# Kernel tuning notes

Measured on AMD Instinct MI355X. Metric: run time of the kernel, lower is better.

The kernel has to match this reference:

```python
import jax, jax.numpy as jnp
import numpy as np

N, E, F, O = 50000, 800000, 128, 128
LOW = [0, 1, 2, 4]           # single-radius (low-pass) channels
BAND = [(0, 1), (1, 2), (2, 4)]  # two-radius (band-pass) channels
KMAX = 4


def setup_inputs() -> dict:
    key = jax.random.key(0)
    ks = jax.random.split(key, 16)
    x = jax.random.normal(ks[0], (N, F), dtype=jnp.float32)
    # edges with no self-loops (dst = src + offset mod N, offset in [1, N))
    src = jax.random.randint(ks[1], (E,), 0, N)
    off = jax.random.randint(ks[2], (E,), 1, N)
    dst = (src + off) % N
    edge_index = jnp.stack([src, dst]).astype(jnp.int64)
    s_lin = 1.0 / np.sqrt(F)
    s_att = 1.0 / np.sqrt(O)
    W_low = jax.random.normal(ks[3], (len(LOW), F, O), jnp.float32) * s_lin
    b_low = jnp.zeros((len(LOW), O), jnp.float32)
    W_band = jax.random.normal(ks[4], (len(BAND), F, O), jnp.float32) * s_lin
    b_band = jnp.zeros((len(BAND), O), jnp.float32)
    att_pre_low = jax.random.normal(ks[5], (1, O), jnp.float32) * s_att
    att_channel_low = jax.random.normal(ks[6], (1, O), jnp.float32) * s_att
    att_pre_band = jax.random.normal(ks[7], (1, O), jnp.float32) * s_att
    att_channel_band = jax.random.normal(ks[8], (1, O), jnp.float32) * s_att
    W_mlp = jax.random.normal(ks[9], (2 * O, O), jnp.float32) * (1.0 / np.sqrt(2 * O))
    b_mlp = jnp.zeros((O,), jnp.float32)
    return {"x": x, "edge_index": edge_index, "W_low": W_low, "b_low": b_low,
            "W_band": W_band, "b_band": b_band,
            "att_pre_low": att_pre_low, "att_channel_low": att_channel_low,
            "att_pre_band": att_pre_band, "att_channel_band": att_channel_band,
            "W_mlp": W_mlp, "b_mlp": b_mlp}


def _sym_norm_weights(src, dst, n, dtype):
    # degree over edges WITHOUT self-loops; self-loop weight is 1, all / 2
    deg = jax.ops.segment_sum(jnp.ones(src.shape[0], dtype), dst, num_segments=n)
    d_inv_sqrt = jnp.where(deg > 0, 1.0 / jnp.sqrt(jnp.maximum(deg, 1e-12)), 0.0)
    return d_inv_sqrt[src] * d_inv_sqrt[dst] * 0.5  # [E]; self-loop coeff is 0.5


def _propagate(x, src, dst, w, n):
    # out[i] = sum_{e: dst=i} w_e * x[src_e] + 0.5 * x[i]  (self-loop term)
    msg = x[src] * w[:, None]  # [E, O]
    return jax.ops.segment_sum(msg, dst, num_segments=n) + 0.5 * x


def _att_combine(h, att_pre, att_ch):
    # h: [C, N, O]; single head attention over channels
    a = jax.nn.relu(h)
    h_pre = a.mean(axis=0)  # [N, O]
    logits = jax.nn.relu(h_pre @ att_pre[0] + jnp.einsum('cno,o->cn', a, att_ch[0]))
    alpha = jax.nn.softmax(logits, axis=0)  # softmax over channels
    return jnp.einsum('cn,cno->no', alpha, h)


def reference(x, edge_index, W_low, b_low, W_band, b_band,
              att_pre_low, att_channel_low, att_pre_band, att_channel_band,
              W_mlp, b_mlp):
    src, dst = edge_index[0], edge_index[1]
    n = x.shape[0]
    w = _sym_norm_weights(src, dst, n, x.dtype)
    # K-hop propagation, store aggregates at required radii
    aggs = {0: x}
    a = x
    for k in range(1, KMAX + 1):
        a = _propagate(a, src, dst, w, n)
        aggs[k] = a
    feats_low = jnp.stack([aggs[k] for k in LOW])                     # [Cl, N, F]
    feats_band = jnp.stack([aggs[k1] - aggs[k2] for k1, k2 in BAND])  # [Cb, N, F]
    h_low = jnp.einsum('cnf,cfo->cno', feats_low, W_low) + b_low[:, None, :]
    h_band = jnp.einsum('cnf,cfo->cno', feats_band, W_band) + b_band[:, None, :]
    out_low = _att_combine(h_low, att_pre_low, att_channel_low)
    out_band = _att_combine(h_band, att_pre_band, att_channel_band)
    out = jnp.concatenate([out_low, out_band], axis=-1) @ W_mlp + b_mlp
    return out
```

## Files before the change

kernel.cpp:

```cpp
#include <hip/hip_runtime.h>
#include <math.h>

#define NN 50000
#define NE 800000
#define TM 16
#define NPAN 4
#define PSZ 12500
#define NT (NN * NPAN)
#define SCH 1024
#define NSB ((NT + SCH - 1) / SCH)

typedef _Float16 half4v __attribute__((ext_vector_type(4)));
typedef _Float16 half8v __attribute__((ext_vector_type(8)));
typedef float f32x4 __attribute__((ext_vector_type(4)));

__device__ __forceinline__ float relu(float v) { return fmaxf(v, 0.0f); }

__global__ __launch_bounds__(256) void k_deg2(const int* __restrict__ ei,
                                              int* __restrict__ deg2) {
  int e = blockIdx.x * 256 + threadIdx.x;
  if (e < NE) {
    int s = ei[e];
    int d = ei[NE + e];
    atomicAdd(&deg2[d * NPAN + s / PSZ], 1);
  }
}

__global__ __launch_bounds__(256) void k_dinv(const int* __restrict__ deg2,
                                              float* __restrict__ dinv) {
  int i = blockIdx.x * 256 + threadIdx.x;
  if (i < NN) {
    int d = deg2[i * NPAN] + deg2[i * NPAN + 1] + deg2[i * NPAN + 2] +
            deg2[i * NPAN + 3];
    dinv[i] = d > 0 ? 1.0f / sqrtf((float)d) : 0.0f;
  }
}

__global__ __launch_bounds__(256) void k_scanA(const int* __restrict__ deg2,
                                               int* __restrict__ bsum) {
  const int tid = threadIdx.x;
  const int lane = tid & 63;
  const int wid = tid >> 6;
  int base = blockIdx.x * SCH + tid * 4;
  int s = 0;
  if (base + 3 < NT) {
    int4 v = *(const int4*)&deg2[base];
    s = v.x + v.y + v.z + v.w;
  } else {
#pragma unroll
    for (int j = 0; j < 4; ++j)
      if (base + j < NT) s += deg2[base + j];
  }
#pragma unroll
  for (int off = 1; off < 64; off <<= 1) s += __shfl_xor(s, off);
  __shared__ int ws[4];
  if (lane == 0) ws[wid] = s;
  __syncthreads();
  if (tid == 0) bsum[blockIdx.x] = ws[0] + ws[1] + ws[2] + ws[3];
}

__global__ __launch_bounds__(256) void k_scanB(const int* __restrict__ bsum,
                                               int* __restrict__ boff,
                                               int* __restrict__ rowptr2) {
  const int tid = threadIdx.x;
  const int lane = tid & 63;
  const int wid = tid >> 6;
  int v = (tid < NSB) ? bsum[tid] : 0;
  int sum = v;
#pragma unroll
  for (int off = 1; off < 64; off <<= 1) {
    int t = __shfl_up(sum, off);
    if (lane >= off) sum += t;
  }
  __shared__ int ws[4];
  if (lane == 63) ws[wid] = sum;
  __syncthreads();
  int wbase = 0;
  for (int w = 0; w < wid; ++w) wbase += ws[w];
  int ex = wbase + sum - v;
  if (tid < NSB) boff[tid] = ex;
  if (tid == NSB - 1) rowptr2[NT] = ex + v;
}

__global__ __launch_bounds__(256) void k_scanC(const int* __restrict__ deg2,
                                               const int* __restrict__ boff,
                                               int* __restrict__ rowptr2) {
  const int tid = threadIdx.x;
  const int lane = tid & 63;
  const int wid = tid >> 6;
  int base = blockIdx.x * SCH + tid * 4;
  int v0 = 0, v1 = 0, v2 = 0, v3 = 0;
  if (base + 3 < NT) {
    int4 v = *(const int4*)&deg2[base];
    v0 = v.x; v1 = v.y; v2 = v.z; v3 = v.w;
  } else {
    if (base + 0 < NT) v0 = deg2[base + 0];
    if (base + 1 < NT) v1 = deg2[base + 1];
    if (base + 2 < NT) v2 = deg2[base + 2];
    if (base + 3 < NT) v3 = deg2[base + 3];
  }
  int tsum = v0 + v1 + v2 + v3;
  int sum = tsum;
#pragma unroll
  for (int off = 1; off < 64; off <<= 1) {
    int t = __shfl_up(sum, off);
    if (lane >= off) sum += t;
  }
  __shared__ int ws[4];
  if (lane == 63) ws[wid] = sum;
  __syncthreads();
  int wbase = 0;
  for (int w = 0; w < wid; ++w) wbase += ws[w];
  int ex = boff[blockIdx.x] + wbase + sum - tsum;
  if (base + 0 < NT) rowptr2[base + 0] = ex;
  if (base + 1 < NT) rowptr2[base + 1] = ex + v0;
  if (base + 2 < NT) rowptr2[base + 2] = ex + v0 + v1;
  if (base + 3 < NT) rowptr2[base + 3] = ex + v0 + v1 + v2;
}

__global__ __launch_bounds__(256) void k_fill(const int* __restrict__ ei,
                                              const float* __restrict__ dinv,
                                              const int* __restrict__ rowptr2,
                                              int* __restrict__ fill2,
                                              int* __restrict__ col,
                                              float* __restrict__ wgt) {
  int e = blockIdx.x * 256 + threadIdx.x;
  if (e < NE) {
    int s = ei[e];
    int d = ei[NE + e];
    float w = dinv[s] * dinv[d] * 0.5f;
    int b = d * NPAN + s / PSZ;
    int pos = rowptr2[b] + atomicAdd(&fill2[b], 1);
    col[pos] = s;
    wgt[pos] = w;
  }
}

__global__ __launch_bounds__(256) void k_x2h(const float* __restrict__ x,
                                             _Float16* __restrict__ xh) {
  int i = blockIdx.x * 256 + threadIdx.x;
  if (i < NN * 32) {
    float4 v = ((const float4*)x)[i];
    half4v h;
    h[0] = (_Float16)v.x; h[1] = (_Float16)v.y;
    h[2] = (_Float16)v.z; h[3] = (_Float16)v.w;
    ((half4v*)xh)[i] = h;
  }
}

__global__ __launch_bounds__(256) void k_hop16(const _Float16* __restrict__ in,
                                               _Float16* __restrict__ out,
                                               const int* __restrict__ rowptr2,
                                               const int* __restrict__ col,
                                               const float* __restrict__ wgt) {
  int g = (blockIdx.x * 256 + threadIdx.x) >> 4;
  int lane = threadIdx.x & 15;
  if (g >= NN) return;
  const half8v* in8 = (const half8v*)in;
  half8v a = in8[(size_t)g * 16 + lane];
  float acc[8];
#pragma unroll
  for (int j = 0; j < 8; ++j) acc[j] = 0.5f * (float)a[j];
  int e0 = rowptr2[g * NPAN];
  int e1 = rowptr2[g * NPAN + NPAN];
  for (int base = e0; base < e1; base += 16) {
    int idx = base + lane;
    int idxc = idx < e1 ? idx : e1 - 1;
    int cv = col[idxc];
    float wv = wgt[idxc];
    int cnt = e1 - base;
    if (cnt > 16) cnt = 16;
    int j = 0;
    for (; j + 4 <= cnt; j += 4) {
      int c0 = __shfl(cv, j, 16), c1 = __shfl(cv, j + 1, 16);
      int c2 = __shfl(cv, j + 2, 16), c3 = __shfl(cv, j + 3, 16);
      float w0 = __shfl(wv, j, 16), w1 = __shfl(wv, j + 1, 16);
      float w2 = __shfl(wv, j + 2, 16), w3 = __shfl(wv, j + 3, 16);
      half8v v0 = in8[(size_t)c0 * 16 + lane];
      half8v v1 = in8[(size_t)c1 * 16 + lane];
      half8v v2 = in8[(size_t)c2 * 16 + lane];
      half8v v3 = in8[(size_t)c3 * 16 + lane];
#pragma unroll
      for (int k = 0; k < 8; ++k)
        acc[k] += w0 * (float)v0[k] + w1 * (float)v1[k] +
                  w2 * (float)v2[k] + w3 * (float)v3[k];
    }
    for (; j < cnt; ++j) {
      int c = __shfl(cv, j, 16);
      float w = __shfl(wv, j, 16);
      half8v v = in8[(size_t)c * 16 + lane];
#pragma unroll
      for (int k = 0; k < 8; ++k) acc[k] += w * (float)v[k];
    }
  }
  half8v r;
#pragma unroll
  for (int j = 0; j < 8; ++j) r[j] = (_Float16)acc[j];
  ((half8v*)out)[(size_t)g * 16 + lane] = r;
}

__global__ __launch_bounds__(256) void k_prep(const float* __restrict__ W_low,
                                              const float* __restrict__ W_band,
                                              const float* __restrict__ W_mlp,
                                              _Float16* __restrict__ WTs) {
  int m = blockIdx.x;
  const float* src;
  if (m < 4)      src = W_low + m * 16384;
  else if (m < 7) src = W_band + (m - 4) * 16384;
  else            src = W_mlp + (m - 7) * 16384;
  _Float16* dst = WTs + (size_t)m * 16384;
  for (int s = threadIdx.x; s < 2048; s += 256) {
    int ct = s >> 8;
    int ks = (s >> 6) & 3;
    int lane = s & 63;
    int mcol = lane & 15, kg = lane >> 4;
    int colc = ct * 16 + mcol;
    int k0 = ks * 32 + 4 * kg;
    _Float16* d = dst + (size_t)s * 8;
#pragma unroll
    for (int j = 0; j < 4; ++j) d[j] = (_Float16)src[(k0 + j) * 128 + colc];
#pragma unroll
    for (int j = 0; j < 4; ++j) d[4 + j] = (_Float16)src[(k0 + 16 + j) * 128 + colc];
  }
}

__global__ __launch_bounds__(256, 3) void k_fused(
    const _Float16* __restrict__ xh, const _Float16* __restrict__ a1,
    const _Float16* __restrict__ a2, const _Float16* __restrict__ a4,
    const _Float16* __restrict__ WTs,
    const float* __restrict__ b_low, const float* __restrict__ b_band,
    const float* __restrict__ apre_l, const float* __restrict__ ach_l,
    const float* __restrict__ apre_b, const float* __restrict__ ach_b,
    const float* __restrict__ b_mlp, float* __restrict__ out) {
  __shared__ _Float16 sH[7][TM][136];
  __shared__ _Float16 sV[TM][264];

  const int tid = threadIdx.x;
  const int wid = tid >> 6;
  const int lane = tid & 63;
  const int mrow = lane & 15;
  const int kg = lane >> 4;
  const int node0 = blockIdx.x * TM;
  const int colw = wid * 32;

  half8v base[4][4];
  {
    const _Float16* arrs[4] = {xh, a1, a2, a4};
#pragma unroll
    for (int t = 0; t < 4; ++t) {
      const _Float16* p = arrs[t] + (size_t)(node0 + mrow) * 128;
#pragma unroll
      for (int ks = 0; ks < 4; ++ks) {
        half4v lo = *(const half4v*)&p[ks * 32 + 4 * kg];
        half4v hi = *(const half4v*)&p[ks * 32 + 4 * kg + 16];
        base[t][ks] = __builtin_shufflevector(lo, hi, 0, 1, 2, 3, 4, 5, 6, 7);
      }
    }
  }

  half8v bfc[8];
  {
    const _Float16* wc = WTs;
#pragma unroll
    for (int ks = 0; ks < 4; ++ks) {
      bfc[ks] = *(const half8v*)&wc[(size_t)(2 * wid) * 2048 + ks * 512 + lane * 8];
      bfc[4 + ks] = *(const half8v*)&wc[(size_t)(2 * wid + 1) * 2048 + ks * 512 + lane * 8];
    }
  }
#pragma unroll
  for (int c = 0; c < 7; ++c) {
    half8v bfn[8];
    if (c < 6) {
      const _Float16* wn = WTs + (size_t)(c + 1) * 16384;
#pragma unroll
      for (int ks = 0; ks < 4; ++ks) {
        bfn[ks] = *(const half8v*)&wn[(size_t)(2 * wid) * 2048 + ks * 512 + lane * 8];
        bfn[4 + ks] = *(const half8v*)&wn[(size_t)(2 * wid + 1) * 2048 + ks * 512 + lane * 8];
      }
    }
    const int ia = (c < 4) ? c : (c - 4);
    const int ib = (c < 4) ? -1 : (c - 3);
    f32x4 acc0 = {0.f, 0.f, 0.f, 0.f}, acc1 = {0.f, 0.f, 0.f, 0.f};
#pragma unroll
    for (int ks = 0; ks < 4; ++ks) {
      half8v af = (ib < 0) ? base[ia][ks] : (base[ia][ks] - base[ib][ks]);
      acc0 = __builtin_amdgcn_mfma_f32_16x16x32_f16(af, bfc[ks], acc0, 0, 0, 0);
      acc1 = __builtin_amdgcn_mfma_f32_16x16x32_f16(af, bfc[4 + ks], acc1, 0, 0, 0);
    }
    const float* bias = (c < 4) ? (b_low + c * 128) : (b_band + (c - 4) * 128);
    float bv0 = bias[colw + mrow];
    float bv1 = bias[colw + 16 + mrow];
#pragma unroll
    for (int r = 0; r < 4; ++r) {
      sH[c][4 * kg + r][colw + mrow] = (_Float16)(acc0[r] + bv0);
      sH[c][4 * kg + r][colw + 16 + mrow] = (_Float16)(acc1[r] + bv1);
    }
    if (c < 6) {
#pragma unroll
      for (int q = 0; q < 8; ++q) bfc[q] = bfn[q];
    }
  }
  __syncthreads();

  {
    const int n = tid >> 4;
    const int cb = (tid & 15) * 8;
    half8v hv[7];
#pragma unroll
    for (int c = 0; c < 7; ++c) hv[c] = *(const half8v*)&sH[c][n][cb];
    float apl[8], acl[8], apb[8], acb[8];
#pragma unroll
    for (int j = 0; j < 8; ++j) {
      apl[j] = apre_l[cb + j]; acl[j] = ach_l[cb + j];
      apb[j] = apre_b[cb + j]; acb[j] = ach_b[cb + j];
    }
    float dpl = 0.f, dpb = 0.f;
    float sarr[7];
#pragma unroll
    for (int c = 0; c < 7; ++c) {
      float sp = 0.f, sc = 0.f;
#pragma unroll
      for (int j = 0; j < 8; ++j) {
        float r = relu((float)hv[c][j]);
        if (c < 4) { sp += r * apl[j]; sc += r * acl[j]; }
        else       { sp += r * apb[j]; sc += r * acb[j]; }
      }
      if (c < 4) dpl += sp; else dpb += sp;
      sarr[c] = sc;
    }
    dpl *= 0.25f;
    dpb *= (1.0f / 3.0f);
#pragma unroll
    for (int m = 1; m <= 8; m <<= 1) {
      dpl += __shfl_xor(dpl, m);
      dpb += __shfl_xor(dpb, m);
#pragma unroll
      for (int c = 0; c < 7; ++c) sarr[c] += __shfl_xor(sarr[c], m);
    }
    float lg[7];
#pragma unroll
    for (int c = 0; c < 7; ++c)
      lg[c] = relu((c < 4 ? dpl : dpb) + sarr[c]);
    float ml = fmaxf(fmaxf(lg[0], lg[1]), fmaxf(lg[2], lg[3]));
    float e0 = expf(lg[0] - ml), e1 = expf(lg[1] - ml);
    float e2 = expf(lg[2] - ml), e3 = expf(lg[3] - ml);
    float invl = 1.0f / (e0 + e1 + e2 + e3);
    float mb = fmaxf(fmaxf(lg[4], lg[5]), lg[6]);
    float f4 = expf(lg[4] - mb), f5 = expf(lg[5] - mb), f6 = expf(lg[6] - mb);
    float invb = 1.0f / (f4 + f5 + f6);
    float al[7];
    al[0] = e0 * invl; al[1] = e1 * invl; al[2] = e2 * invl; al[3] = e3 * invl;
    al[4] = f4 * invb; al[5] = f5 * invb; al[6] = f6 * invb;
    half8v vl8, vb8;
#pragma unroll
    for (int j = 0; j < 8; ++j) {
      float vl = 0.f, vb = 0.f;
#pragma unroll
      for (int c = 0; c < 4; ++c) vl += al[c] * (float)hv[c][j];
#pragma unroll
      for (int c = 4; c < 7; ++c) vb += al[c] * (float)hv[c][j];
      vl8[j] = (_Float16)vl;
      vb8[j] = (_Float16)vb;
    }
    *(half8v*)&sV[n][cb] = vl8;
    *(half8v*)&sV[n][128 + cb] = vb8;
  }
  __syncthreads();

  f32x4 m0 = {0.f, 0.f, 0.f, 0.f}, m1 = {0.f, 0.f, 0.f, 0.f};
#pragma unroll
  for (int hh = 0; hh < 2; ++hh) {
    const _Float16* wm = WTs + (size_t)(7 + hh) * 16384;
#pragma unroll
    for (int ks = 0; ks < 4; ++ks) {
      int ka = hh * 128 + ks * 32 + 4 * kg;
      half4v aa = *(const half4v*)&sV[mrow][ka];
      half4v ab = *(const half4v*)&sV[mrow][ka + 16];
      half8v af = __builtin_shufflevector(aa, ab, 0, 1, 2, 3, 4, 5, 6, 7);
      half8v bf0 = *(const half8v*)&wm[(size_t)(2 * wid) * 2048 + ks * 512 + lane * 8];
      half8v bf1 = *(const half8v*)&wm[(size_t)(2 * wid + 1) * 2048 + ks * 512 + lane * 8];
      m0 = __builtin_amdgcn_mfma_f32_16x16x32_f16(af, bf0, m0, 0, 0, 0);
      m1 = __builtin_amdgcn_mfma_f32_16x16x32_f16(af, bf1, m1, 0, 0, 0);
    }
  }
  float bm0 = b_mlp[colw + mrow];
  float bm1 = b_mlp[colw + 16 + mrow];
#pragma unroll
  for (int r = 0; r < 4; ++r) {
    out[(size_t)(node0 + 4 * kg + r) * 128 + colw + mrow] = m0[r] + bm0;
    out[(size_t)(node0 + 4 * kg + r) * 128 + colw + 16 + mrow] = m1[r] + bm1;
  }
}

extern "C" void kernel_launch(void* const* d_in, const int* in_sizes, int n_in,
                              void* d_out, int out_size, void* d_ws, size_t ws_size,
                              hipStream_t stream) {
  const float* x      = (const float*)d_in[0];
  const int* ei       = (const int*)d_in[1];
  const float* W_low  = (const float*)d_in[2];
  const float* b_low  = (const float*)d_in[3];
  const float* W_band = (const float*)d_in[4];
  const float* b_band = (const float*)d_in[5];
  const float* apre_l = (const float*)d_in[6];
  const float* ach_l  = (const float*)d_in[7];
  const float* apre_b = (const float*)d_in[8];
  const float* ach_b  = (const float*)d_in[9];
  const float* W_mlp  = (const float*)d_in[10];
  const float* b_mlp  = (const float*)d_in[11];
  float* out = (float*)d_out;

  char* ws = (char*)d_ws;
  size_t off = 0;
  auto take = [&](size_t bytes) -> void* {
    void* p = ws + off;
    off = (off + bytes + 255) & ~(size_t)255;
    return p;
  };
  int*   deg2   = (int*)take((size_t)NT * 4);
  int*   fill2  = (int*)take((size_t)NT * 4);
  size_t zero_bytes = off;
  float* dinv   = (float*)take((size_t)NN * 4);
  int*   rowptr2 = (int*)take((size_t)(NT + 1) * 4);
  int*   bsum   = (int*)take((size_t)NSB * 4);
  int*   boff   = (int*)take((size_t)NSB * 4);
  int*   col    = (int*)take((size_t)NE * 4);
  float* wgt    = (float*)take((size_t)NE * 4);
  _Float16* xh  = (_Float16*)take((size_t)NN * 128 * 2);
  _Float16* a1h = (_Float16*)take((size_t)NN * 128 * 2);
  _Float16* a2h = (_Float16*)take((size_t)NN * 128 * 2);
  _Float16* a3h = (_Float16*)take((size_t)NN * 128 * 2);
  _Float16* a4h = (_Float16*)take((size_t)NN * 128 * 2);
  _Float16* WTs = (_Float16*)take((size_t)9 * 16384 * 2);
  (void)ws_size; (void)in_sizes; (void)n_in; (void)out_size;

  hipMemsetAsync(d_ws, 0, zero_bytes, stream);
  k_prep<<<9, 256, 0, stream>>>(W_low, W_band, W_mlp, WTs);
  k_x2h<<<(NN * 32 + 255) / 256, 256, 0, stream>>>(x, xh);
  k_deg2<<<(NE + 255) / 256, 256, 0, stream>>>(ei, deg2);
  k_dinv<<<(NN + 255) / 256, 256, 0, stream>>>(deg2, dinv);
  k_scanA<<<NSB, 256, 0, stream>>>(deg2, bsum);
  k_scanB<<<1, 256, 0, stream>>>(bsum, boff, rowptr2);
  k_scanC<<<NSB, 256, 0, stream>>>(deg2, boff, rowptr2);
  k_fill<<<(NE + 255) / 256, 256, 0, stream>>>(ei, dinv, rowptr2, fill2, col, wgt);
  k_hop16<<<(NN * 16 + 255) / 256, 256, 0, stream>>>(xh,  a1h, rowptr2, col, wgt);
  k_hop16<<<(NN * 16 + 255) / 256, 256, 0, stream>>>(a1h, a2h, rowptr2, col, wgt);
  k_hop16<<<(NN * 16 + 255) / 256, 256, 0, stream>>>(a2h, a3h, rowptr2, col, wgt);
  k_hop16<<<(NN * 16 + 255) / 256, 256, 0, stream>>>(a3h, a4h, rowptr2, col, wgt);
  k_fused<<<NN / TM, 256, 0, stream>>>(xh, a1h, a2h, a4h, WTs, b_low, b_band,
                                       apre_l, ach_l, apre_b, ach_b, b_mlp, out);
}
```

Measured before the change: 300.2 us.

## Degree-sort nodes for hop load balance and double fused tile to 32 rows

Adds a degree histogram, a prefix scan and a scatter that build a node permutation ordered by in-degree. The hop kernels use it so that the 16-lane groups sharing a wavefront handle nodes of similar degree, which is meant to reduce divergence and imbalance in the gather loop. Separately, the fused projection/attention/MLP kernel now processes 32 nodes per block, so each weight fragment is reused across two row tiles and streamed per channel instead of double-buffered in registers. The cost is three extra small kernels, an extra indirection in each hop, lost locality of output writes in the hop kernels, and a changed register and occupancy profile in the fused kernel.

```diff
diff --git a/kernel.cpp b/kernel.cpp
--- a/kernel.cpp
+++ b/kernel.cpp
@@ -3,7 +3,7 @@
 
 #define NN 50000
 #define NE 800000
-#define TM 16
+#define TM 32
 #define NPAN 4
 #define PSZ 12500
 #define NT (NN * NPAN)
@@ -33,6 +33,43 @@
     int d = deg2[i * NPAN] + deg2[i * NPAN + 1] + deg2[i * NPAN + 2] +
             deg2[i * NPAN + 3];
     dinv[i] = d > 0 ? 1.0f / sqrtf((float)d) : 0.0f;
+  }
+}
+
+__global__ __launch_bounds__(256) void k_hist(const int* __restrict__ deg2,
+                                              int* __restrict__ hist) {
+  int i = blockIdx.x * 256 + threadIdx.x;
+  if (i < NN) {
+    int d = deg2[i * NPAN] + deg2[i * NPAN + 1] + deg2[i * NPAN + 2] +
+            deg2[i * NPAN + 3];
+    atomicAdd(&hist[d < 63 ? d : 63], 1);
+  }
+}
+
+__global__ __launch_bounds__(64) void k_binscan(const int* __restrict__ hist,
+                                                int* __restrict__ binoff) {
+  int lane = threadIdx.x;
+  int v = hist[lane];
+  int sum = v;
+#pragma unroll
+  for (int off = 1; off < 64; off <<= 1) {
+    int t = __shfl_up(sum, off);
+    if (lane >= off) sum += t;
+  }
+  binoff[lane] = sum - v;
+}
+
+__global__ __launch_bounds__(256) void k_scatter(const int* __restrict__ deg2,
+                                                 const int* __restrict__ binoff,
+                                                 int* __restrict__ binfill,
+                                                 int* __restrict__ perm) {
+  int i = blockIdx.x * 256 + threadIdx.x;
+  if (i < NN) {
+    int d = deg2[i * NPAN] + deg2[i * NPAN + 1] + deg2[i * NPAN + 2] +
+            deg2[i * NPAN + 3];
+    int b = d < 63 ? d : 63;
+    int pos = binoff[b] + atomicAdd(&binfill[b], 1);
+    perm[pos] = i;
   }
 }
 
@@ -152,10 +189,12 @@
                                                _Float16* __restrict__ out,
                                                const int* __restrict__ rowptr2,
                                                const int* __restrict__ col,
-                                               const float* __restrict__ wgt) {
-  int g = (blockIdx.x * 256 + threadIdx.x) >> 4;
+                                               const float* __restrict__ wgt,
+                                               const int* __restrict__ perm) {
+  int idx = (blockIdx.x * 256 + threadIdx.x) >> 4;
   int lane = threadIdx.x & 15;
-  if (g >= NN) return;
+  if (idx >= NN) return;
+  int g = perm[idx];
   const half8v* in8 = (const half8v*)in;
   half8v a = in8[(size_t)g * 16 + lane];
   float acc[8];
@@ -164,10 +203,10 @@
   int e0 = rowptr2[g * NPAN];
   int e1 = rowptr2[g * NPAN + NPAN];
   for (int base = e0; base < e1; base += 16) {
-    int idx = base + lane;
-    int idxc = idx < e1 ? idx : e1 - 1;
-    int cv = col[idxc];
-    float wv = wgt[idxc];
+    int idq = base + lane;
+    int idqc = idq < e1 ? idq : e1 - 1;
+    int cv = col[idqc];
+    float wv = wgt[idqc];
     int cnt = e1 - base;
     if (cnt > 16) cnt = 16;
     int j = 0;
@@ -224,7 +263,48 @@
   }
 }
 
-__global__ __launch_bounds__(256, 3) void k_fused(
+#define LOADF2(d0, d1, src)                                                    \
+  {                                                                            \
+    const _Float16* p0_ = (src) + (size_t)(node0 + mrow) * 128;                \
+    const _Float16* p1_ = (src) + (size_t)row1 * 128;                          \
+    _Pragma("unroll")                                                          \
+    for (int ks = 0; ks < 4; ++ks) {                                           \
+      half4v lo_ = *(const half4v*)&p0_[ks * 32 + 4 * kg];                     \
+      half4v hi_ = *(const half4v*)&p0_[ks * 32 + 4 * kg + 16];                \
+      d0[ks] = __builtin_shufflevector(lo_, hi_, 0, 1, 2, 3, 4, 5, 6, 7);      \
+      half4v l2_ = *(const half4v*)&p1_[ks * 32 + 4 * kg];                     \
+      half4v h2_ = *(const half4v*)&p1_[ks * 32 + 4 * kg + 16];                \
+      d1[ks] = __builtin_shufflevector(l2_, h2_, 0, 1, 2, 3, 4, 5, 6, 7);      \
+    }                                                                          \
+  }
+
+#define CH2(c, AE0, AE1, BIASPTR)                                              \
+  {                                                                            \
+    const _Float16* wc_ = WTs + (size_t)(c) * 16384;                           \
+    f32x4 A00_ = {0.f,0.f,0.f,0.f}, A01_ = {0.f,0.f,0.f,0.f};                  \
+    f32x4 A10_ = {0.f,0.f,0.f,0.f}, A11_ = {0.f,0.f,0.f,0.f};                  \
+    _Pragma("unroll")                                                          \
+    for (int ks = 0; ks < 4; ++ks) {                                           \
+      half8v b0_ = *(const half8v*)&wc_[(size_t)(2 * wid) * 2048 + ks * 512 + lane * 8];     \
+      half8v b1_ = *(const half8v*)&wc_[(size_t)(2 * wid + 1) * 2048 + ks * 512 + lane * 8]; \
+      half8v af0_ = (AE0);                                                     \
+      half8v af1_ = (AE1);                                                     \
+      A00_ = __builtin_amdgcn_mfma_f32_16x16x32_f16(af0_, b0_, A00_, 0, 0, 0); \
+      A01_ = __builtin_amdgcn_mfma_f32_16x16x32_f16(af0_, b1_, A01_, 0, 0, 0); \
+      A10_ = __builtin_amdgcn_mfma_f32_16x16x32_f16(af1_, b0_, A10_, 0, 0, 0); \
+      A11_ = __builtin_amdgcn_mfma_f32_16x16x32_f16(af1_, b1_, A11_, 0, 0, 0); \
+    }                                                                          \
+    float bv0_ = (BIASPTR)[colw + mrow], bv1_ = (BIASPTR)[colw + 16 + mrow];   \
+    _Pragma("unroll")                                                          \
+    for (int r = 0; r < 4; ++r) {                                              \
+      sH[c][4 * kg + r][colw + mrow] = (_Float16)(A00_[r] + bv0_);             \
+      sH[c][4 * kg + r][colw + 16 + mrow] = (_Float16)(A01_[r] + bv1_);        \
+      sH[c][16 + 4 * kg + r][colw + mrow] = (_Float16)(A10_[r] + bv0_);        \
+      sH[c][16 + 4 * kg + r][colw + 16 + mrow] = (_Float16)(A11_[r] + bv1_);   \
+    }                                                                          \
+  }
+
+__global__ __launch_bounds__(256) void k_fused(
     const _Float16* __restrict__ xh, const _Float16* __restrict__ a1,
     const _Float16* __restrict__ a2, const _Float16* __restrict__ a4,
     const _Float16* __restrict__ WTs,
@@ -242,153 +322,125 @@
   const int kg = lane >> 4;
   const int node0 = blockIdx.x * TM;
   const int colw = wid * 32;
-
-  half8v base[4][4];
+  int row1 = node0 + 16 + mrow;
+  if (row1 >= NN) row1 = NN - 1;
+
+  half8v fa0[4], fa1[4], fb0[4], fb1[4];
+
+  LOADF2(fa0, fa1, xh);
+  CH2(0, fa0[ks], fa1[ks], b_low + 0 * 128);
+  LOADF2(fb0, fb1, a1);
+  CH2(4, fa0[ks] - fb0[ks], fa1[ks] - fb1[ks], b_band + 0 * 128);
+  CH2(1, fb0[ks], fb1[ks], b_low + 1 * 128);
+  LOADF2(fa0, fa1, a2);
+  CH2(5, fb0[ks] - fa0[ks], fb1[ks] - fa1[ks], b_band + 1 * 128);
+  CH2(2, fa0[ks], fa1[ks], b_low + 2 * 128);
+  LOADF2(fb0, fb1, a4);
+  CH2(6, fa0[ks] - fb0[ks], fa1[ks] - fb1[ks], b_band + 2 * 128);
+  CH2(3, fb0[ks], fb1[ks], b_low + 3 * 128);
+  __syncthreads();
+
   {
-    const _Float16* arrs[4] = {xh, a1, a2, a4};
-#pragma unroll
-    for (int t = 0; t < 4; ++t) {
-      const _Float16* p = arrs[t] + (size_t)(node0 + mrow) * 128;
-#pragma unroll
-      for (int ks = 0; ks < 4; ++ks) {
-        half4v lo = *(const half4v*)&p[ks * 32 + 4 * kg];
-        half4v hi = *(const half4v*)&p[ks * 32 + 4 * kg + 16];
-        base[t][ks] = __builtin_shufflevector(lo, hi, 0, 1, 2, 3, 4, 5, 6, 7);
-      }
-    }
-  }
-
-  half8v bfc[8];
-  {
-    const _Float16* wc = WTs;
-#pragma unroll
-    for (int ks = 0; ks < 4; ++ks) {
-      bfc[ks] = *(const half8v*)&wc[(size_t)(2 * wid) * 2048 + ks * 512 + lane * 8];
-      bfc[4 + ks] = *(const half8v*)&wc[(size_t)(2 * wid + 1) * 2048 + ks * 512 + lane * 8];
-    }
-  }
-#pragma unroll
-  for (int c = 0; c < 7; ++c) {
-    half8v bfn[8];
-    if (c < 6) {
-      const _Float16* wn = WTs + (size_t)(c + 1) * 16384;
-#pragma unroll
-      for (int ks = 0; ks < 4; ++ks) {
-        bfn[ks] = *(const half8v*)&wn[(size_t)(2 * wid) * 2048 + ks * 512 + lane * 8];
-        bfn[4 + ks] = *(const half8v*)&wn[(size_t)(2 * wid + 1) * 2048 + ks * 512 + lane * 8];
-      }
-    }
-    const int ia = (c < 4) ? c : (c - 4);
-    const int ib = (c < 4) ? -1 : (c - 3);
-    f32x4 acc0 = {0.f, 0.f, 0.f, 0.f}, acc1 = {0.f, 0.f, 0.f, 0.f};
-#pragma unroll
-    for (int ks = 0; ks < 4; ++ks) {
-      half8v af = (ib < 0) ? base[ia][ks] : (base[ia][ks] - base[ib][ks]);
-      acc0 = __builtin_amdgcn_mfma_f32_16x16x32_f16(af, bfc[ks], acc0, 0, 0, 0);
-      acc1 = __builtin_amdgcn_mfma_f32_16x16x32_f16(af, bfc[4 + ks], acc1, 0, 0, 0);
-    }
-    const float* bias = (c < 4) ? (b_low + c * 128) : (b_band + (c - 4) * 128);
-    float bv0 = bias[colw + mrow];
-    float bv1 = bias[colw + 16 + mrow];
-#pragma unroll
-    for (int r = 0; r < 4; ++r) {
-      sH[c][4 * kg + r][colw + mrow] = (_Float16)(acc0[r] + bv0);
-      sH[c][4 * kg + r][colw + 16 + mrow] = (_Float16)(acc1[r] + bv1);
-    }
-    if (c < 6) {
-#pragma unroll
-      for (int q = 0; q < 8; ++q) bfc[q] = bfn[q];
-    }
-  }
-  __syncthreads();
-
-  {
-    const int n = tid >> 4;
     const int cb = (tid & 15) * 8;
-    half8v hv[7];
-#pragma unroll
-    for (int c = 0; c < 7; ++c) hv[c] = *(const half8v*)&sH[c][n][cb];
     float apl[8], acl[8], apb[8], acb[8];
 #pragma unroll
     for (int j = 0; j < 8; ++j) {
       apl[j] = apre_l[cb + j]; acl[j] = ach_l[cb + j];
       apb[j] = apre_b[cb + j]; acb[j] = ach_b[cb + j];
     }
-    float dpl = 0.f, dpb = 0.f;
-    float sarr[7];
-#pragma unroll
-    for (int c = 0; c < 7; ++c) {
-      float sp = 0.f, sc = 0.f;
+#pragma unroll
+    for (int s = 0; s < 2; ++s) {
+      const int n = (tid >> 4) + 16 * s;
+      half8v hv[7];
+#pragma unroll
+      for (int c = 0; c < 7; ++c) hv[c] = *(const half8v*)&sH[c][n][cb];
+      float dpl = 0.f, dpb = 0.f;
+      float sarr[7];
+#pragma unroll
+      for (int c = 0; c < 7; ++c) {
+        float sp = 0.f, sc = 0.f;
+#pragma unroll
+        for (int j = 0; j < 8; ++j) {
+          float r = relu((float)hv[c][j]);
+          if (c < 4) { sp += r * apl[j]; sc += r * acl[j]; }
+          else       { sp += r * apb[j]; sc += r * acb[j]; }
+        }
+        if (c < 4) dpl += sp; else dpb += sp;
+        sarr[c] = sc;
+      }
+      dpl *= 0.25f;
+      dpb *= (1.0f / 3.0f);
+#pragma unroll
+      for (int m = 1; m <= 8; m <<= 1) {
+        dpl += __shfl_xor(dpl, m);
+        dpb += __shfl_xor(dpb, m);
+#pragma unroll
+        for (int c = 0; c < 7; ++c) sarr[c] += __shfl_xor(sarr[c], m);
+      }
+      float lg[7];
+#pragma unroll
+      for (int c = 0; c < 7; ++c)
+        lg[c] = relu((c < 4 ? dpl : dpb) + sarr[c]);
+      float ml = fmaxf(fmaxf(lg[0], lg[1]), fmaxf(lg[2], lg[3]));
+      float e0 = expf(lg[0] - ml), e1 = expf(lg[1] - ml);
+      float e2 = expf(lg[2] - ml), e3 = expf(lg[3] - ml);
+      float invl = 1.0f / (e0 + e1 + e2 + e3);
+      float mb = fmaxf(fmaxf(lg[4], lg[5]), lg[6]);
+      float f4 = expf(lg[4] - mb), f5 = expf(lg[5] - mb), f6 = expf(lg[6] - mb);
+      float invb = 1.0f / (f4 + f5 + f6);
+      float al[7];
+      al[0] = e0 * invl; al[1] = e1 * invl; al[2] = e2 * invl; al[3] = e3 * invl;
+      al[4] = f4 * invb; al[5] = f5 * invb; al[6] = f6 * invb;
+      half8v vl8, vb8;
 #pragma unroll
       for (int j = 0; j < 8; ++j) {
-        float r = relu((float)hv[c][j]);
-        if (c < 4) { sp += r * apl[j]; sc += r * acl[j]; }
-        else       { sp += r * apb[j]; sc += r * acb[j]; }
+        float vl = 0.f, vb = 0.f;
+#pragma unroll
+        for (int c = 0; c < 4; ++c) vl += al[c] * (float)hv[c][j];
+#pragma unroll
+        for (int c = 4; c < 7; ++c) vb += al[c] * (float)hv[c][j];
+        vl8[j] = (_Float16)vl;
+        vb8[j] = (_Float16)vb;
       }
-      if (c < 4) dpl += sp; else dpb += sp;
-      sarr[c] = sc;
+      *(half8v*)&sV[n][cb] = vl8;
+      *(half8v*)&sV[n][128 + cb] = vb8;
     }
-    dpl *= 0.25f;
-    dpb *= (1.0f / 3.0f);
-#pragma unroll
-    for (int m = 1; m <= 8; m <<= 1) {
-      dpl += __shfl_xor(dpl, m);
-      dpb += __shfl_xor(dpb, m);
-#pragma unroll
-      for (int c = 0; c < 7; ++c) sarr[c] += __shfl_xor(sarr[c], m);
-    }
-    float lg[7];
-#pragma unroll
-    for (int c = 0; c < 7; ++c)
-      lg[c] = relu((c < 4 ? dpl : dpb) + sarr[c]);
-    float ml = fmaxf(fmaxf(lg[0], lg[1]), fmaxf(lg[2], lg[3]));
-    float e0 = expf(lg[0] - ml), e1 = expf(lg[1] - ml);
-    float e2 = expf(lg[2] - ml), e3 = expf(lg[3] - ml);
-    float invl = 1.0f / (e0 + e1 + e2 + e3);
-    float mb = fmaxf(fmaxf(lg[4], lg[5]), lg[6]);
-    float f4 = expf(lg[4] - mb), f5 = expf(lg[5] - mb), f6 = expf(lg[6] - mb);
-    float invb = 1.0f / (f4 + f5 + f6);
-    float al[7];
-    al[0] = e0 * invl; al[1] = e1 * invl; al[2] = e2 * invl; al[3] = e3 * invl;
-    al[4] = f4 * invb; al[5] = f5 * invb; al[6] = f6 * invb;
-    half8v vl8, vb8;
-#pragma unroll
-    for (int j = 0; j < 8; ++j) {
-      float vl = 0.f, vb = 0.f;
-#pragma unroll
-      for (int c = 0; c < 4; ++c) vl += al[c] * (float)hv[c][j];
-#pragma unroll
-      for (int c = 4; c < 7; ++c) vb += al[c] * (float)hv[c][j];
-      vl8[j] = (_Float16)vl;
-      vb8[j] = (_Float16)vb;
-    }
-    *(half8v*)&sV[n][cb] = vl8;
-    *(half8v*)&sV[n][128 + cb] = vb8;
   }
   __syncthreads();
 
-  f32x4 m0 = {0.f, 0.f, 0.f, 0.f}, m1 = {0.f, 0.f, 0.f, 0.f};
+  f32x4 m00 = {0.f,0.f,0.f,0.f}, m01 = {0.f,0.f,0.f,0.f};
+  f32x4 m10 = {0.f,0.f,0.f,0.f}, m11 = {0.f,0.f,0.f,0.f};
 #pragma unroll
   for (int hh = 0; hh < 2; ++hh) {
     const _Float16* wm = WTs + (size_t)(7 + hh) * 16384;
 #pragma unroll
     for (int ks = 0; ks < 4; ++ks) {
       int ka = hh * 128 + ks * 32 + 4 * kg;
-      half4v aa = *(const half4v*)&sV[mrow][ka];
-      half4v ab = *(const half4v*)&sV[mrow][ka + 16];
-      half8v af = __builtin_shufflevector(aa, ab, 0, 1, 2, 3, 4, 5, 6, 7);
-      half8v bf0 = *(const half8v*)&wm[(size_t)(2 * wid) * 2048 + ks * 512 + lane * 8];
-      half8v bf1 = *(const half8v*)&wm[(size_t)(2 * wid + 1) * 2048 + ks * 512 + lane * 8];
-      m0 = __builtin_amdgcn_mfma_f32_16x16x32_f16(af, bf0, m0, 0, 0, 0);
-      m1 = __builtin_amdgcn_mfma_f32_16x16x32_f16(af, bf1, m1, 0, 0, 0);
+      half8v b0 = *(const half8v*)&wm[(size_t)(2 * wid) * 2048 + ks * 512 + lane * 8];
+      half8v b1 = *(const half8v*)&wm[(size_t)(2 * wid + 1) * 2048 + ks * 512 + lane * 8];
+      half4v a0a = *(const half4v*)&sV[mrow][ka];
+      half4v a0b = *(const half4v*)&sV[mrow][ka + 16];
+      half8v af0 = __builtin_shufflevector(a0a, a0b, 0, 1, 2, 3, 4, 5, 6, 7);
+      half4v a1a = *(const half4v*)&sV[16 + mrow][ka];
+      half4v a1b = *(const half4v*)&sV[16 + mrow][ka + 16];
+      half8v af1 = __builtin_shufflevector(a1a, a1b, 0, 1, 2, 3, 4, 5, 6, 7);
+      m00 = __builtin_amdgcn_mfma_f32_16x16x32_f16(af0, b0, m00, 0, 0, 0);
+      m01 = __builtin_amdgcn_mfma_f32_16x16x32_f16(af0, b1, m01, 0, 0, 0);
+      m10 = __builtin_amdgcn_mfma_f32_16x16x32_f16(af1, b0, m10, 0, 0, 0);
+      m11 = __builtin_amdgcn_mfma_f32_16x16x32_f16(af1, b1, m11, 0, 0, 0);
     }
   }
   float bm0 = b_mlp[colw + mrow];
   float bm1 = b_mlp[colw + 16 + mrow];
 #pragma unroll
   for (int r = 0; r < 4; ++r) {
-    out[(size_t)(node0 + 4 * kg + r) * 128 + colw + mrow] = m0[r] + bm0;
-    out[(size_t)(node0 + 4 * kg + r) * 128 + colw + 16 + mrow] = m1[r] + bm1;
+    out[(size_t)(node0 + 4 * kg + r) * 128 + colw + mrow] = m00[r] + bm0;
+    out[(size_t)(node0 + 4 * kg + r) * 128 + colw + 16 + mrow] = m01[r] + bm1;
+    int n1 = node0 + 16 + 4 * kg + r;
+    if (n1 < NN) {
+      out[(size_t)n1 * 128 + colw + mrow] = m10[r] + bm0;
+      out[(size_t)n1 * 128 + colw + 16 + mrow] = m11[r] + bm1;
+    }
   }
 }
 
@@ -416,15 +468,19 @@
     off = (off + bytes + 255) & ~(size_t)255;
     return p;
   };
-  int*   deg2   = (int*)take((size_t)NT * 4);
-  int*   fill2  = (int*)take((size_t)NT * 4);
+  int*   deg2    = (int*)take((size_t)NT * 4);
+  int*   fill2   = (int*)take((size_t)NT * 4);
+  int*   hist    = (int*)take((size_t)64 * 4);
+  int*   binfill = (int*)take((size_t)64 * 4);
   size_t zero_bytes = off;
-  float* dinv   = (float*)take((size_t)NN * 4);
+  float* dinv    = (float*)take((size_t)NN * 4);
   int*   rowptr2 = (int*)take((size_t)(NT + 1) * 4);
-  int*   bsum   = (int*)take((size_t)NSB * 4);
-  int*   boff   = (int*)take((size_t)NSB * 4);
-  int*   col    = (int*)take((size_t)NE * 4);
-  float* wgt    = (float*)take((size_t)NE * 4);
+  int*   bsum    = (int*)take((size_t)NSB * 4);
+  int*   boff    = (int*)take((size_t)NSB * 4);
+  int*   binoff  = (int*)take((size_t)64 * 4);
+  int*   perm    = (int*)take((size_t)NN * 4);
+  int*   col     = (int*)take((size_t)NE * 4);
+  float* wgt     = (float*)take((size_t)NE * 4);
   _Float16* xh  = (_Float16*)take((size_t)NN * 128 * 2);
   _Float16* a1h = (_Float16*)take((size_t)NN * 128 * 2);
   _Float16* a2h = (_Float16*)take((size_t)NN * 128 * 2);
@@ -438,14 +494,17 @@
   k_x2h<<<(NN * 32 + 255) / 256, 256, 0, stream>>>(x, xh);
   k_deg2<<<(NE + 255) / 256, 256, 0, stream>>>(ei, deg2);
   k_dinv<<<(NN + 255) / 256, 256, 0, stream>>>(deg2, dinv);
+  k_hist<<<(NN + 255) / 256, 256, 0, stream>>>(deg2, hist);
+  k_binscan<<<1, 64, 0, stream>>>(hist, binoff);
+  k_scatter<<<(NN + 255) / 256, 256, 0, stream>>>(deg2, binoff, binfill, perm);
   k_scanA<<<NSB, 256, 0, stream>>>(deg2, bsum);
   k_scanB<<<1, 256, 0, stream>>>(bsum, boff, rowptr2);
   k_scanC<<<NSB, 256, 0, stream>>>(deg2, boff, rowptr2);
   k_fill<<<(NE + 255) / 256, 256, 0, stream>>>(ei, dinv, rowptr2, fill2, col, wgt);
-  k_hop16<<<(NN * 16 + 255) / 256, 256, 0, stream>>>(xh,  a1h, rowptr2, col, wgt);
-  k_hop16<<<(NN * 16 + 255) / 256, 256, 0, stream>>>(a1h, a2h, rowptr2, col, wgt);
-  k_hop16<<<(NN * 16 + 255) / 256, 256, 0, stream>>>(a2h, a3h, rowptr2, col, wgt);
-  k_hop16<<<(NN * 16 + 255) / 256, 256, 0, stream>>>(a3h, a4h, rowptr2, col, wgt);
-  k_fused<<<NN / TM, 256, 0, stream>>>(xh, a1h, a2h, a4h, WTs, b_low, b_band,
-                                       apre_l, ach_l, apre_b, ach_b, b_mlp, out);
-}
+  k_hop16<<<(NN * 16 + 255) / 256, 256, 0, stream>>>(xh,  a1h, rowptr2, col, wgt, perm);
+  k_hop16<<<(NN * 16 + 255) / 256, 256, 0, stream>>>(a1h, a2h, rowptr2, col, wgt, perm);
+  k_hop16<<<(NN * 16 + 255) / 256, 256, 0, stream>>>(a2h, a3h, rowptr2, col, wgt, perm);
+  k_hop16<<<(NN * 16 + 255) / 256, 256, 0, stream>>>(a3h, a4h, rowptr2, col, wgt, perm);
+  k_fused<<<(NN + TM - 1) / TM, 256, 0, stream>>>(xh, a1h, a2h, a4h, WTs, b_low, b_band,
+                                                  apre_l, ach_l, apre_b, ach_b, b_mlp, out);
+}
```

Result: slower. 591.0 us (+96.9%).
